# Performance work log

Hardware: AMD Instinct MI355X
Metric: run time of the kernel (lower is better)

Reference implementation:

```python
import jax, jax.numpy as jnp
import numpy as np

B, T, D = 4, 4096, 256
N_SCALES, N_EXPERTS = 3, 4
KERNELS = [5, 9, 17]           # kernel bank, one group of N_EXPERTS experts per size
E = N_SCALES * N_EXPERTS       # 12 total experts
EPS = 1e-5


def _dw_causal_conv(x, w):
    """Depthwise causal conv over time. x:[B,T,D], w:[k,D] -> [B,T,D]."""
    k = w.shape[0]
    xp = jnp.pad(x, ((0, 0), (k - 1, 0), (0, 0)))
    return jax.lax.conv_general_dilated(
        xp, w[:, None, :], window_strides=(1,), padding='VALID',
        dimension_numbers=('NWC', 'WIO', 'NWC'), feature_group_count=x.shape[-1])


def setup_inputs() -> dict:
    key = jax.random.key(0)
    ks = jax.random.split(key, 12)
    s = 0.02
    return {
        'x':       jax.random.normal(ks[0], (B, T, D), jnp.float32),
        'conv_k5':  jax.random.normal(ks[1], (N_EXPERTS, 5, D), jnp.float32) * s,
        'conv_k9':  jax.random.normal(ks[2], (N_EXPERTS, 9, D), jnp.float32) * s,
        'conv_k17': jax.random.normal(ks[3], (N_EXPERTS, 17, D), jnp.float32) * s,
        'proj_W':   jax.random.normal(ks[4], (E, D, D), jnp.float32) * s,
        'proj_b':   jnp.zeros((E, D), jnp.float32),
        'router_W': jax.random.normal(ks[5], (D, E), jnp.float32) * s,
        'router_b': jnp.zeros((E,), jnp.float32),
        'out_W':    jax.random.normal(ks[6], (D, D), jnp.float32) * s,
        'out_b':    jnp.zeros((D,), jnp.float32),
        'gamma':    jnp.ones((D,), jnp.float32),
        'beta':     jnp.zeros((D,), jnp.float32),
    }


def reference(x, conv_k5, conv_k9, conv_k17, proj_W, proj_b,
              router_W, router_b, out_W, out_b, gamma, beta):
    # per-scale expert SSM (causal depthwise conv), vmapped over the 4 experts per size
    ssm_out = jnp.concatenate([
        jax.vmap(lambda w: _dw_causal_conv(x, w))(conv_k5),
        jax.vmap(lambda w: _dw_causal_conv(x, w))(conv_k9),
        jax.vmap(lambda w: _dw_causal_conv(x, w))(conv_k17),
    ], axis=0)                                             # [E,B,T,D]
    # per-expert linear projection -> [B,T,E,D]
    stack = jnp.einsum('ebtd,edf->btef', ssm_out, proj_W) + proj_b
    # router: convex combination over E experts per token
    weights = jax.nn.softmax(x @ router_W + router_b, axis=-1)   # [B,T,E]
    mixed = jnp.einsum('btef,bte->btf', stack, weights)          # [B,T,D]
    # LayerNorm
    mu = jnp.mean(mixed, axis=-1, keepdims=True)
    var = jnp.var(mixed, axis=-1, keepdims=True)
    normed = (mixed - mu) * jax.lax.rsqrt(var + EPS) * gamma + beta
    return normed @ out_W + out_b
```

## Files before the change

### kernel.cpp

```cpp
#include <hip/hip_runtime.h>
#include <hip/hip_bf16.h>

typedef short short8 __attribute__((ext_vector_type(8)));
typedef short short4_t __attribute__((ext_vector_type(4)));
typedef float floatx4 __attribute__((ext_vector_type(4)));

#define DEVI __device__ __forceinline__


DEVI float bf2f(__hip_bfloat16 v) { return __bfloat162float(v); }
DEVI __hip_bfloat16 f2bf(float v) { return __float2bfloat16(v); }
DEVI unsigned short bfbits(float v) { __hip_bfloat16 b = f2bf(v); return *(unsigned short*)&b; }

__global__ __launch_bounds__(256) void prep_kernel(
    const float* __restrict__ rW,
    const float* __restrict__ projW,
    const float* __restrict__ outW,
    const float* __restrict__ projb,
    __hip_bfloat16* __restrict__ projWT,
    __hip_bfloat16* __restrict__ outWT,
    __hip_bfloat16* __restrict__ projbT,
    __hip_bfloat16* __restrict__ rWT)
{
    __shared__ __align__(16) __hip_bfloat16 Tt[64 * 72];
    const int bid = blockIdx.x;
    const int tid = threadIdx.x;

    if (bid == 208) {
#pragma unroll
        for (int k = 0; k < 32; k++)
            projbT[tid * 32 + k] = (k < 12) ? f2bf(projb[k * 256 + tid]) : f2bf(0.f);
#pragma unroll
        for (int e = 0; e < 16; e++)
            rWT[e * 256 + tid] = (e < 12) ? f2bf(rW[tid * 12 + e]) : f2bf(0.f);
        return;
    }
    const float* src;
    __hip_bfloat16* dst;
    if (bid < 192) {
        int e = bid >> 4, ti = (bid & 15) >> 2, tj = bid & 3;
        src = projW + (e << 16) + (ti * 64) * 256 + tj * 64;
        dst = projWT + (e << 16) + (tj * 64) * 256 + ti * 64;
    } else {
        int b3 = bid - 192, ti = b3 >> 2, tj = b3 & 3;
        src = outW + (ti * 64) * 256 + tj * 64;
        dst = outWT + (tj * 64) * 256 + ti * 64;
    }
#pragma unroll
    for (int i = 0; i < 4; i++) {
        int r = i * 16 + (tid >> 4);
        int c4 = (tid & 15) * 4;
        float4 f = *(const float4*)(src + r * 256 + c4);
        Tt[(c4 + 0) * 72 + r] = f2bf(f.x);
        Tt[(c4 + 1) * 72 + r] = f2bf(f.y);
        Tt[(c4 + 2) * 72 + r] = f2bf(f.z);
        Tt[(c4 + 3) * 72 + r] = f2bf(f.w);
    }
    __syncthreads();
#pragma unroll
    for (int i = 0; i < 2; i++) {
        int c = i * 32 + (tid >> 3);
        int r8 = (tid & 7) * 8;
        *(short8*)(dst + c * 256 + r8) = *(const short8*)(Tt + c * 72 + r8);
    }
}


template<int K>
DEVI void conv_reg(const float2 (&cf)[17], const unsigned (&xr)[32],
                   const float4 (&wt4)[4], unsigned* __restrict__ dp)
{
    constexpr int OFF = 17 - K;
#pragma unroll
    for (int t = 0; t < 16; t++) {
        float y0 = 0.f, y1 = 0.f;
#pragma unroll
        for (int i = 0; i < K; i++) {
            unsigned u = xr[t + OFF + i];
            y0 = fmaf(cf[i].x, __uint_as_float(u << 16), y0);
            y1 = fmaf(cf[i].y, __uint_as_float(u & 0xffff0000u), y1);
        }
        float wt = wt4[t >> 2][t & 3];
        unsigned pv = ((unsigned)bfbits(y1 * wt) << 16) | (unsigned)bfbits(y0 * wt);
        dp[t * 132] = pv;
    }
}

template<int NKS>
DEVI void gemm_pre(const __hip_bfloat16* __restrict__ A, int astride,
                   const short8 (&B)[4][2], floatx4 (&acc)[4][2],
                   int l16, int quad)
{
    const __hip_bfloat16* ap = A + l16 * astride + quad * 8;
    short8 a[4];
#pragma unroll
    for (int mf = 0; mf < 4; mf++) a[mf] = *(const short8*)(ap + mf * 16 * astride);
#pragma unroll
    for (int ks = 0; ks < NKS; ks++) {
        short8 na[4];
        if (ks < NKS - 1) {
#pragma unroll
            for (int mf = 0; mf < 4; mf++)
                na[mf] = *(const short8*)(ap + mf * 16 * astride + (ks + 1) * 32);
        }
#pragma unroll
        for (int nt = 0; nt < 2; nt++)
#pragma unroll
            for (int mf = 0; mf < 4; mf++)
                acc[mf][nt] = __builtin_amdgcn_mfma_f32_16x16x32_bf16(
                    a[mf], B[ks][nt], acc[mf][nt], 0, 0, 0);
        if (ks < NKS - 1) {
#pragma unroll
            for (int mf = 0; mf < 4; mf++) a[mf] = na[mf];
        }
    }
}

__global__ __launch_bounds__(512, 1) void fused_kernel(
    const float* __restrict__ x,
    const float* __restrict__ ck5, const float* __restrict__ ck9,
    const float* __restrict__ ck17,
    const float* __restrict__ rb,
    const float* __restrict__ gmm, const float* __restrict__ bta,
    const float* __restrict__ outb,
    const __hip_bfloat16* __restrict__ projWT,
    const __hip_bfloat16* __restrict__ outWT,
    const __hip_bfloat16* __restrict__ projbT,
    const __hip_bfloat16* __restrict__ rWT,
    float* __restrict__ out)
{
    __shared__ __align__(16) char smem[50432];
    __hip_bfloat16* xs = (__hip_bfloat16*)smem;
    __hip_bfloat16* As = (__hip_bfloat16*)smem;
    __hip_bfloat16* normed = (__hip_bfloat16*)smem;
    float* wts_s = (float*)(smem + 42240);
    float* psum  = (float*)(smem + 45312);
    float* psq   = (float*)(smem + 47616);
    float* muA   = (float*)(smem + 49920);
    float* rsA   = (float*)(smem + 50176);

    const int tid  = threadIdx.x;
    const int wave = tid >> 6;
    const int lane = tid & 63;
    const int quad = lane >> 4;
    const int l16  = lane & 15;
    const int nsl  = wave * 32;
    const int m0   = blockIdx.x * 64;
    const int bb   = m0 >> 12;
    const int t0   = m0 & 4095;

    {
        const float* xb = x + (size_t)bb * 4096 * 256;
        for (int idx = tid; idx < 80 * 64; idx += 512) {
            int row = idx >> 6, c4 = (idx & 63) << 2;
            int gt = t0 - 16 + row;
            short4_t v = {0, 0, 0, 0};
            if (gt >= 0) {
                float4 f = *(const float4*)(xb + (size_t)gt * 256 + c4);
                v[0] = (short)bfbits(f.x); v[1] = (short)bfbits(f.y);
                v[2] = (short)bfbits(f.z); v[3] = (short)bfbits(f.w);
            }
            *(short4_t*)(xs + row * 264 + c4) = v;
        }
    }
    __syncthreads();

    if (wave < 4) {
        floatx4 ra = {0.f, 0.f, 0.f, 0.f};
        const __hip_bfloat16* ap = xs + (16 + wave * 16 + l16) * 264 + quad * 8;
        const __hip_bfloat16* bp = rWT + l16 * 256 + quad * 8;
#pragma unroll
        for (int kk = 0; kk < 256; kk += 32)
            ra = __builtin_amdgcn_mfma_f32_16x16x32_bf16(
                *(const short8*)(ap + kk), *(const short8*)(bp + kk), ra, 0, 0, 0);
        float rbv = (l16 < 12) ? rb[l16] : 0.f;
#pragma unroll
        for (int r = 0; r < 4; r++) {
            float v = (l16 < 12) ? (ra[r] + rbv) : -1e30f;
            float mx = v;
            mx = fmaxf(mx, __shfl_xor(mx, 1));
            mx = fmaxf(mx, __shfl_xor(mx, 2));
            mx = fmaxf(mx, __shfl_xor(mx, 4));
            mx = fmaxf(mx, __shfl_xor(mx, 8));
            float ex = (l16 < 12) ? __expf(v - mx) : 0.f;
            float sm = ex;
            sm += __shfl_xor(sm, 1);
            sm += __shfl_xor(sm, 2);
            sm += __shfl_xor(sm, 4);
            sm += __shfl_xor(sm, 8);
            if (l16 < 12) wts_s[l16 * 64 + (wave * 16 + quad * 4 + r)] = ex / sm;
        }
    }

    const int d0   = 2 * (tid & 127);
    const int tloc = (tid >> 7) * 16;
    unsigned xr[32];
#pragma unroll
    for (int j = 0; j < 32; j++)
        xr[j] = *(const unsigned*)(xs + (tloc + j) * 264 + d0);
    __syncthreads();

    auto loadCoef = [&](float2 (&cf)[17], int e) {
        if (e < 4) {
            const float* cw = ck5 + e * 5 * 256;
#pragma unroll
            for (int j = 0; j < 17; j++)
                cf[j] = (j < 5) ? *(const float2*)(cw + j * 256 + d0) : make_float2(0.f, 0.f);
        } else if (e < 8) {
            const float* cw = ck9 + (e - 4) * 9 * 256;
#pragma unroll
            for (int j = 0; j < 17; j++)
                cf[j] = (j < 9) ? *(const float2*)(cw + j * 256 + d0) : make_float2(0.f, 0.f);
        } else {
            const float* cw = ck17 + (e - 8) * 17 * 256;
#pragma unroll
            for (int j = 0; j < 17; j++)
                cf[j] = *(const float2*)(cw + j * 256 + d0);
        }
    };
    auto loadB8 = [&](short8 (&B)[4][2], const __hip_bfloat16* base, int rs, int kstep) {
#pragma unroll
        for (int ks = 0; ks < 4; ks++)
#pragma unroll
            for (int nt = 0; nt < 2; nt++)
                B[ks][nt] = *(const short8*)(base + nt * 16 * rs + ks * kstep);
    };
    auto produce = [&](int e, const float2 (&cf)[17]) {
        float4 wt4[4];
#pragma unroll
        for (int g = 0; g < 4; g++)
            wt4[g] = *(const float4*)(wts_s + e * 64 + tloc + 4 * g);
        unsigned* dp = (unsigned*)As + tloc * 132 + (d0 >> 1);
        if (e < 4)      conv_reg<5>(cf, xr, wt4, dp);
        else if (e < 8) conv_reg<9>(cf, xr, wt4, dp);
        else            conv_reg<17>(cf, xr, wt4, dp);
    };
    auto produceBias = [&]() {
        int t = tid >> 3, k4 = (tid & 7) * 4;
        short4_t v;
#pragma unroll
        for (int j = 0; j < 4; j++) {
            int k = k4 + j;
            v[j] = (k < 12) ? (short)bfbits(wts_s[k * 64 + t]) : (short)0;
        }
        *(short4_t*)(As + t * 264 + k4) = v;
    };

    floatx4 acc[4][2];
#pragma unroll
    for (int i = 0; i < 4; i++)
#pragma unroll
        for (int j = 0; j < 2; j++) acc[i][j] = {0.f, 0.f, 0.f, 0.f};

    float2 cf[17];
    short8 BA[4][2], BB[4][2];

    loadCoef(cf, 0);
    loadB8(BA, projWT + (0 << 16) + 0   + (nsl + l16) * 256 + quad * 8, 256, 32);
    loadB8(BB, projWT + (0 << 16) + 128 + (nsl + l16) * 256 + quad * 8, 256, 32);
    produce(0, cf);
    __syncthreads();

#pragma unroll 1
    for (int c = 0; c < 12; c++) {
        if (c < 11) loadCoef(cf, c + 1);
        gemm_pre<4>(As, 264, BA, acc, l16, quad);
        gemm_pre<4>(As + 128, 264, BB, acc, l16, quad);
        if (c < 11) {
            int e = c + 1;
            loadB8(BA, projWT + (e << 16) + 0   + (nsl + l16) * 256 + quad * 8, 256, 32);
            loadB8(BB, projWT + (e << 16) + 128 + (nsl + l16) * 256 + quad * 8, 256, 32);
        } else {
            loadB8(BA, projbT + (nsl + l16) * 32 + quad * 8, 32, 0);
        }
        __syncthreads();
        if (c < 11) produce(c + 1, cf);
        else        produceBias();
        __syncthreads();
    }
    gemm_pre<1>(As, 264, BA, acc, l16, quad);

    loadB8(BA, outWT + 0   + (nsl + l16) * 256 + quad * 8, 256, 32);
    loadB8(BB, outWT + 128 + (nsl + l16) * 256 + quad * 8, 256, 32);

    {
        float s[16], s2[16];
#pragma unroll
        for (int mf = 0; mf < 4; mf++)
#pragma unroll
            for (int r = 0; r < 4; r++) {
                int i = mf * 4 + r;
                float v = 0.f, q = 0.f;
#pragma unroll
                for (int nt = 0; nt < 2; nt++) {
                    float a = acc[mf][nt][r];
                    v += a; q += a * a;
                }
                s[i] = v; s2[i] = q;
            }
#pragma unroll
        for (int m = 1; m <= 8; m <<= 1)
#pragma unroll
            for (int i = 0; i < 16; i++) {
                s[i]  += __shfl_xor(s[i], m);
                s2[i] += __shfl_xor(s2[i], m);
            }
#pragma unroll
        for (int i = 0; i < 16; i++)
            if (l16 == i) {
                int row = (i >> 2) * 16 + quad * 4 + (i & 3);
                psum[row * 9 + wave] = s[i];
                psq[row * 9 + wave]  = s2[i];
            }
    }
    __syncthreads();
    if (tid < 64) {
        float ss = 0.f, qq = 0.f;
#pragma unroll
        for (int p = 0; p < 8; p++) { ss += psum[tid * 9 + p]; qq += psq[tid * 9 + p]; }
        float mu = ss * 0.00390625f;
        float var = fmaxf(qq * 0.00390625f - mu * mu, 0.f);
        muA[tid] = mu;
        rsA[tid] = rsqrtf(var + 1e-5f);
    }
    __syncthreads();

#pragma unroll
    for (int nt = 0; nt < 2; nt++) {
        int col = nsl + nt * 16 + l16;
        float g = gmm[col], bt = bta[col];
#pragma unroll
        for (int mf = 0; mf < 4; mf++)
#pragma unroll
            for (int r = 0; r < 4; r++) {
                int row = mf * 16 + quad * 4 + r;
                normed[row * 264 + col] =
                    f2bf((acc[mf][nt][r] - muA[row]) * rsA[row] * g + bt);
            }
    }
    __syncthreads();

    floatx4 acc2[4][2];
#pragma unroll
    for (int i = 0; i < 4; i++)
#pragma unroll
        for (int j = 0; j < 2; j++) acc2[i][j] = {0.f, 0.f, 0.f, 0.f};
    gemm_pre<4>(normed, 264, BA, acc2, l16, quad);
    gemm_pre<4>(normed + 128, 264, BB, acc2, l16, quad);

    float* op = out + (size_t)m0 * 256;
#pragma unroll
    for (int nt = 0; nt < 2; nt++) {
        int col = nsl + nt * 16 + l16;
        float ob = outb[col];
#pragma unroll
        for (int mf = 0; mf < 4; mf++)
#pragma unroll
            for (int r = 0; r < 4; r++) {
                int row = mf * 16 + quad * 4 + r;
                op[row * 256 + col] = acc2[mf][nt][r] + ob;
            }
    }
}

extern "C" void kernel_launch(void* const* d_in, const int* in_sizes, int n_in,
                              void* d_out, int out_size, void* d_ws, size_t ws_size,
                              hipStream_t stream)
{
    (void)in_sizes; (void)n_in; (void)out_size; (void)ws_size;
    const float* x     = (const float*)d_in[0];
    const float* ck5   = (const float*)d_in[1];
    const float* ck9   = (const float*)d_in[2];
    const float* ck17  = (const float*)d_in[3];
    const float* projW = (const float*)d_in[4];
    const float* projb = (const float*)d_in[5];
    const float* rW    = (const float*)d_in[6];
    const float* rb    = (const float*)d_in[7];
    const float* outW  = (const float*)d_in[8];
    const float* outb  = (const float*)d_in[9];
    const float* gmm   = (const float*)d_in[10];
    const float* bta   = (const float*)d_in[11];

    __hip_bfloat16* projWT = (__hip_bfloat16*)d_ws;
    __hip_bfloat16* outWT  = (__hip_bfloat16*)((char*)d_ws + 1572864);
    __hip_bfloat16* projbT = (__hip_bfloat16*)((char*)d_ws + 1703936);
    __hip_bfloat16* rWT    = (__hip_bfloat16*)((char*)d_ws + 1720320);

    prep_kernel<<<dim3(209), dim3(256), 0, stream>>>(
        rW, projW, outW, projb, projWT, outWT, projbT, rWT);
    fused_kernel<<<dim3(256), dim3(512), 0, stream>>>(
        x, ck5, ck9, ck17, rb, gmm, bta, outb,
        projWT, outWT, projbT, rWT, (float*)d_out);
}
```

Baseline: 165.6 us.

## Double-buffer expert activations and interleave conv production with MFMA GEMM

Replaces the single shared activation buffer with two ping-pong buffers. While MFMAs consume the current expert's conv output, the conv for the next expert is computed and written into the other buffer. Each expert step now needs one barrier instead of two, and VALU conv work is interleaved with matrix ops. In exchange, dynamic shared memory grows to about 84 KB and register pressure rises, and the kernel now depends on setting the dynamic-LDS attribute.

```diff
diff --git a/kernel.cpp b/kernel.cpp
--- a/kernel.cpp
+++ b/kernel.cpp
@@ -65,6 +65,7 @@
     }
 }
 
+constexpr int SMEM_BYTES = 84224;
 
 template<int K>
 DEVI void conv_reg(const float2 (&cf)[17], const unsigned (&xr)[32],
@@ -83,6 +84,57 @@
         float wt = wt4[t >> 2][t & 3];
         unsigned pv = ((unsigned)bfbits(y1 * wt) << 16) | (unsigned)bfbits(y0 * wt);
         dp[t * 132] = pv;
+    }
+}
+
+template<int K>
+DEVI void chunk_fused(const __hip_bfloat16* __restrict__ bufC,
+                      unsigned* __restrict__ dpN,
+                      const short8 (&BA)[4][2], const short8 (&BB)[4][2],
+                      floatx4 (&acc)[4][2],
+                      const float2 (&cf)[17], const unsigned (&xr)[32],
+                      const float4 (&wt4)[4],
+                      int l16, int quad)
+{
+    constexpr int OFF = 17 - K;
+    const __hip_bfloat16* ap = bufC + l16 * 264 + quad * 8;
+    short8 a[4];
+#pragma unroll
+    for (int mf = 0; mf < 4; mf++) a[mf] = *(const short8*)(ap + mf * 16 * 264);
+#pragma unroll
+    for (int ks = 0; ks < 8; ks++) {
+#pragma unroll
+        for (int j = 0; j < 2; j++) {
+            int t = 2 * ks + j;
+            float y0 = 0.f, y1 = 0.f;
+#pragma unroll
+            for (int i = 0; i < K; i++) {
+                unsigned u = xr[t + OFF + i];
+                y0 = fmaf(cf[i].x, __uint_as_float(u << 16), y0);
+                y1 = fmaf(cf[i].y, __uint_as_float(u & 0xffff0000u), y1);
+            }
+            float wt = wt4[t >> 2][t & 3];
+            unsigned pv = ((unsigned)bfbits(y1 * wt) << 16) | (unsigned)bfbits(y0 * wt);
+            dpN[t * 132] = pv;
+        }
+        short8 na[4];
+        if (ks < 7) {
+#pragma unroll
+            for (int mf = 0; mf < 4; mf++)
+                na[mf] = *(const short8*)(ap + mf * 16 * 264 + (ks + 1) * 32);
+        }
+#pragma unroll
+        for (int nt = 0; nt < 2; nt++) {
+            short8 b = (ks < 4) ? BA[ks][nt] : BB[ks - 4][nt];
+#pragma unroll
+            for (int mf = 0; mf < 4; mf++)
+                acc[mf][nt] = __builtin_amdgcn_mfma_f32_16x16x32_bf16(
+                    a[mf], b, acc[mf][nt], 0, 0, 0);
+        }
+        if (ks < 7) {
+#pragma unroll
+            for (int mf = 0; mf < 4; mf++) a[mf] = na[mf];
+        }
     }
 }
 
@@ -129,15 +181,15 @@
     const __hip_bfloat16* __restrict__ rWT,
     float* __restrict__ out)
 {
-    __shared__ __align__(16) char smem[50432];
-    __hip_bfloat16* xs = (__hip_bfloat16*)smem;
-    __hip_bfloat16* As = (__hip_bfloat16*)smem;
-    __hip_bfloat16* normed = (__hip_bfloat16*)smem;
-    float* wts_s = (float*)(smem + 42240);
-    float* psum  = (float*)(smem + 45312);
-    float* psq   = (float*)(smem + 47616);
-    float* muA   = (float*)(smem + 49920);
-    float* rsA   = (float*)(smem + 50176);
+    extern __shared__ char smem[];
+    __hip_bfloat16* xs   = (__hip_bfloat16*)smem;
+    __hip_bfloat16* bufA = (__hip_bfloat16*)smem;
+    __hip_bfloat16* bufB = (__hip_bfloat16*)(smem + 42240);
+    float* wts_s = (float*)(smem + 76032);
+    float* psum  = (float*)(smem + 79104);
+    float* psq   = (float*)(smem + 81408);
+    float* muA   = (float*)(smem + 83712);
+    float* rsA   = (float*)(smem + 83968);
 
     const int tid  = threadIdx.x;
     const int wave = tid >> 6;
@@ -225,17 +277,12 @@
             for (int nt = 0; nt < 2; nt++)
                 B[ks][nt] = *(const short8*)(base + nt * 16 * rs + ks * kstep);
     };
-    auto produce = [&](int e, const float2 (&cf)[17]) {
-        float4 wt4[4];
+    auto loadWt = [&](float4 (&w)[4], int e) {
 #pragma unroll
         for (int g = 0; g < 4; g++)
-            wt4[g] = *(const float4*)(wts_s + e * 64 + tloc + 4 * g);
-        unsigned* dp = (unsigned*)As + tloc * 132 + (d0 >> 1);
-        if (e < 4)      conv_reg<5>(cf, xr, wt4, dp);
-        else if (e < 8) conv_reg<9>(cf, xr, wt4, dp);
-        else            conv_reg<17>(cf, xr, wt4, dp);
+            w[g] = *(const float4*)(wts_s + e * 64 + tloc + 4 * g);
     };
-    auto produceBias = [&]() {
+    auto produceBias = [&](__hip_bfloat16* dst) {
         int t = tid >> 3, k4 = (tid & 7) * 4;
         short4_t v;
 #pragma unroll
@@ -243,7 +290,7 @@
             int k = k4 + j;
             v[j] = (k < 12) ? (short)bfbits(wts_s[k * 64 + t]) : (short)0;
         }
-        *(short4_t*)(As + t * 264 + k4) = v;
+        *(short4_t*)(dst + t * 264 + k4) = v;
     };
 
     floatx4 acc[4][2];
@@ -254,33 +301,50 @@
 
     float2 cf[17];
     short8 BA[4][2], BB[4][2];
+    __hip_bfloat16* bufC = bufA;
+    __hip_bfloat16* bufN = bufB;
 
     loadCoef(cf, 0);
-    loadB8(BA, projWT + (0 << 16) + 0   + (nsl + l16) * 256 + quad * 8, 256, 32);
-    loadB8(BB, projWT + (0 << 16) + 128 + (nsl + l16) * 256 + quad * 8, 256, 32);
-    produce(0, cf);
-    __syncthreads();
+    loadB8(BA, projWT + (nsl + l16) * 256 + quad * 8, 256, 32);
+    loadB8(BB, projWT + 128 + (nsl + l16) * 256 + quad * 8, 256, 32);
+    {
+        float4 wt4[4];
+        loadWt(wt4, 0);
+        unsigned* dp = (unsigned*)bufC + tloc * 132 + (d0 >> 1);
+        conv_reg<5>(cf, xr, wt4, dp);
+    }
+    __syncthreads();
+
+#define REGION(KP, EXPERT)                                                      \
+    {                                                                           \
+        const int e_ = (EXPERT);                                                \
+        loadCoef(cf, e_);                                                       \
+        float4 wt4[4];                                                          \
+        loadWt(wt4, e_);                                                        \
+        unsigned* dpN = (unsigned*)bufN + tloc * 132 + (d0 >> 1);               \
+        chunk_fused<KP>(bufC, dpN, BA, BB, acc, cf, xr, wt4, l16, quad);        \
+        loadB8(BA, projWT + ((size_t)e_ << 16) + (nsl + l16) * 256 + quad * 8, 256, 32); \
+        loadB8(BB, projWT + ((size_t)e_ << 16) + 128 + (nsl + l16) * 256 + quad * 8, 256, 32); \
+        { __hip_bfloat16* t_ = bufC; bufC = bufN; bufN = t_; }                  \
+        __syncthreads();                                                        \
+    }
 
 #pragma unroll 1
-    for (int c = 0; c < 12; c++) {
-        if (c < 11) loadCoef(cf, c + 1);
-        gemm_pre<4>(As, 264, BA, acc, l16, quad);
-        gemm_pre<4>(As + 128, 264, BB, acc, l16, quad);
-        if (c < 11) {
-            int e = c + 1;
-            loadB8(BA, projWT + (e << 16) + 0   + (nsl + l16) * 256 + quad * 8, 256, 32);
-            loadB8(BB, projWT + (e << 16) + 128 + (nsl + l16) * 256 + quad * 8, 256, 32);
-        } else {
-            loadB8(BA, projbT + (nsl + l16) * 32 + quad * 8, 32, 0);
-        }
-        __syncthreads();
-        if (c < 11) produce(c + 1, cf);
-        else        produceBias();
-        __syncthreads();
-    }
-    gemm_pre<1>(As, 264, BA, acc, l16, quad);
-
-    loadB8(BA, outWT + 0   + (nsl + l16) * 256 + quad * 8, 256, 32);
+    for (int r = 0; r < 3; r++)  REGION(5,  r + 1)
+#pragma unroll 1
+    for (int r = 3; r < 7; r++)  REGION(9,  r + 1)
+#pragma unroll 1
+    for (int r = 7; r < 11; r++) REGION(17, r + 1)
+#undef REGION
+
+    produceBias(bufN);
+    gemm_pre<4>(bufC, 264, BA, acc, l16, quad);
+    gemm_pre<4>(bufC + 128, 264, BB, acc, l16, quad);
+    loadB8(BA, projbT + (nsl + l16) * 32 + quad * 8, 32, 0);
+    __syncthreads();
+    gemm_pre<1>(bufN, 264, BA, acc, l16, quad);
+
+    loadB8(BA, outWT + (nsl + l16) * 256 + quad * 8, 256, 32);
     loadB8(BB, outWT + 128 + (nsl + l16) * 256 + quad * 8, 256, 32);
 
     {
@@ -325,6 +389,7 @@
     }
     __syncthreads();
 
+    __hip_bfloat16* normed = bufC;
 #pragma unroll
     for (int nt = 0; nt < 2; nt++) {
         int col = nsl + nt * 16 + l16;
@@ -386,9 +451,16 @@
     __hip_bfloat16* projbT = (__hip_bfloat16*)((char*)d_ws + 1703936);
     __hip_bfloat16* rWT    = (__hip_bfloat16*)((char*)d_ws + 1720320);
 
+    static bool attr_set = false;
+    if (!attr_set) {
+        hipFuncSetAttribute((const void*)fused_kernel,
+                            hipFuncAttributeMaxDynamicSharedMemorySize, SMEM_BYTES);
+        attr_set = true;
+    }
+
     prep_kernel<<<dim3(209), dim3(256), 0, stream>>>(
         rW, projW, outW, projb, projWT, outWT, projbT, rWT);
-    fused_kernel<<<dim3(256), dim3(512), 0, stream>>>(
+    fused_kernel<<<dim3(256), dim3(512), SMEM_BYTES, stream>>>(
         x, ck5, ck9, ck17, rb, gmm, bta, outb,
         projWT, outWT, projbT, rWT, (float*)d_out);
 }
```

After: 168.9 us. 2.0% more time.

## Double-buffer expert conv tiles and split waves between GEMM-first and conv-first order

Applied to the files above, without the earlier changes.

The per-expert loop now keeps the conv output in two LDS buffers and ping-pongs between them, so the conv for expert r+1 can overlap the MFMA GEMM for expert r. Half the waves issue the GEMM first and the other half issue the conv first, which staggers MFMA and VALU work. The conv now reads x from LDS through a sliding register window instead of holding 32 preloaded registers, and GEMM B operands stream from global memory inside the k-loop instead of being fully preloaded. Dynamic shared memory grows to about 118 KB, and the extra global B loads in the inner loop may add latency.

```diff
diff --git a/kernel.cpp b/kernel.cpp
--- a/kernel.cpp
+++ b/kernel.cpp
@@ -65,53 +65,70 @@
     }
 }
 
+constexpr int SMEM_BYTES = 118016;
 
 template<int K>
-DEVI void conv_reg(const float2 (&cf)[17], const unsigned (&xr)[32],
-                   const float4 (&wt4)[4], unsigned* __restrict__ dp)
+DEVI void conv_lds2(const float2 (&cf)[17], const unsigned* __restrict__ xsu,
+                    int tloc, int du, const float4 (&wt4)[4],
+                    unsigned* __restrict__ dp)
 {
-    constexpr int OFF = 17 - K;
+    unsigned w[16];
+#pragma unroll
+    for (int i = 0; i < K - 1; i++)
+        w[i] = xsu[(16 + tloc - (K - 1) + i) * 132 + du];
 #pragma unroll
     for (int t = 0; t < 16; t++) {
-        float y0 = 0.f, y1 = 0.f;
-#pragma unroll
-        for (int i = 0; i < K; i++) {
-            unsigned u = xr[t + OFF + i];
-            y0 = fmaf(cf[i].x, __uint_as_float(u << 16), y0);
-            y1 = fmaf(cf[i].y, __uint_as_float(u & 0xffff0000u), y1);
+        unsigned nv = xsu[(16 + tloc + t) * 132 + du];
+        float y0 = cf[K - 1].x * __uint_as_float(nv << 16);
+        float y1 = cf[K - 1].y * __uint_as_float(nv & 0xffff0000u);
+#pragma unroll
+        for (int i = 0; i < K - 1; i++) {
+            y0 = fmaf(cf[i].x, __uint_as_float(w[i] << 16), y0);
+            y1 = fmaf(cf[i].y, __uint_as_float(w[i] & 0xffff0000u), y1);
         }
         float wt = wt4[t >> 2][t & 3];
         unsigned pv = ((unsigned)bfbits(y1 * wt) << 16) | (unsigned)bfbits(y0 * wt);
         dp[t * 132] = pv;
+#pragma unroll
+        for (int i = 0; i + 1 < K - 1; i++) w[i] = w[i + 1];
+        if (K > 1) w[K - 2] = nv;
     }
 }
 
 template<int NKS>
-DEVI void gemm_pre(const __hip_bfloat16* __restrict__ A, int astride,
-                   const short8 (&B)[4][2], floatx4 (&acc)[4][2],
-                   int l16, int quad)
+DEVI void gemm_inl(const __hip_bfloat16* __restrict__ A, int astride,
+                   const __hip_bfloat16* __restrict__ Bg, int bstride,
+                   floatx4 (&acc)[4][2], int l16, int quad, int nsl)
 {
     const __hip_bfloat16* ap = A + l16 * astride + quad * 8;
-    short8 a[4];
+    const __hip_bfloat16* bp = Bg + (nsl + l16) * bstride + quad * 8;
+    short8 a[4], b[2];
 #pragma unroll
     for (int mf = 0; mf < 4; mf++) a[mf] = *(const short8*)(ap + mf * 16 * astride);
 #pragma unroll
+    for (int nt = 0; nt < 2; nt++) b[nt] = *(const short8*)(bp + nt * 16 * bstride);
+#pragma unroll
     for (int ks = 0; ks < NKS; ks++) {
-        short8 na[4];
+        short8 na[4], nb[2];
         if (ks < NKS - 1) {
 #pragma unroll
             for (int mf = 0; mf < 4; mf++)
                 na[mf] = *(const short8*)(ap + mf * 16 * astride + (ks + 1) * 32);
+#pragma unroll
+            for (int nt = 0; nt < 2; nt++)
+                nb[nt] = *(const short8*)(bp + nt * 16 * bstride + (ks + 1) * 32);
         }
 #pragma unroll
         for (int nt = 0; nt < 2; nt++)
 #pragma unroll
             for (int mf = 0; mf < 4; mf++)
                 acc[mf][nt] = __builtin_amdgcn_mfma_f32_16x16x32_bf16(
-                    a[mf], B[ks][nt], acc[mf][nt], 0, 0, 0);
+                    a[mf], b[nt], acc[mf][nt], 0, 0, 0);
         if (ks < NKS - 1) {
 #pragma unroll
             for (int mf = 0; mf < 4; mf++) a[mf] = na[mf];
+#pragma unroll
+            for (int nt = 0; nt < 2; nt++) b[nt] = nb[nt];
         }
     }
 }
@@ -129,15 +146,16 @@
     const __hip_bfloat16* __restrict__ rWT,
     float* __restrict__ out)
 {
-    __shared__ __align__(16) char smem[50432];
-    __hip_bfloat16* xs = (__hip_bfloat16*)smem;
-    __hip_bfloat16* As = (__hip_bfloat16*)smem;
-    __hip_bfloat16* normed = (__hip_bfloat16*)smem;
-    float* wts_s = (float*)(smem + 42240);
-    float* psum  = (float*)(smem + 45312);
-    float* psq   = (float*)(smem + 47616);
-    float* muA   = (float*)(smem + 49920);
-    float* rsA   = (float*)(smem + 50176);
+    extern __shared__ char smem[];
+    __hip_bfloat16* xs   = (__hip_bfloat16*)smem;
+    __hip_bfloat16* bufA = (__hip_bfloat16*)(smem + 42240);
+    __hip_bfloat16* bufB = (__hip_bfloat16*)(smem + 76032);
+    float* wts_s = (float*)(smem + 109824);
+    float* psum  = (float*)(smem + 112896);
+    float* psq   = (float*)(smem + 115200);
+    float* muA   = (float*)(smem + 117504);
+    float* rsA   = (float*)(smem + 117760);
+    const unsigned* xsu = (const unsigned*)xs;
 
     const int tid  = threadIdx.x;
     const int wave = tid >> 6;
@@ -145,6 +163,7 @@
     const int quad = lane >> 4;
     const int l16  = lane & 15;
     const int nsl  = wave * 32;
+    const bool gemmFirst = (wave >= 4);
     const int m0   = blockIdx.x * 64;
     const int bb   = m0 >> 12;
     const int t0   = m0 & 4095;
@@ -191,14 +210,11 @@
             if (l16 < 12) wts_s[l16 * 64 + (wave * 16 + quad * 4 + r)] = ex / sm;
         }
     }
+    __syncthreads();
 
     const int d0   = 2 * (tid & 127);
+    const int du   = d0 >> 1;
     const int tloc = (tid >> 7) * 16;
-    unsigned xr[32];
-#pragma unroll
-    for (int j = 0; j < 32; j++)
-        xr[j] = *(const unsigned*)(xs + (tloc + j) * 264 + d0);
-    __syncthreads();
 
     auto loadCoef = [&](float2 (&cf)[17], int e) {
         if (e < 4) {
@@ -218,24 +234,19 @@
                 cf[j] = *(const float2*)(cw + j * 256 + d0);
         }
     };
-    auto loadB8 = [&](short8 (&B)[4][2], const __hip_bfloat16* base, int rs, int kstep) {
-#pragma unroll
-        for (int ks = 0; ks < 4; ks++)
-#pragma unroll
-            for (int nt = 0; nt < 2; nt++)
-                B[ks][nt] = *(const short8*)(base + nt * 16 * rs + ks * kstep);
-    };
-    auto produce = [&](int e, const float2 (&cf)[17]) {
+    auto produce = [&](int e, __hip_bfloat16* dst) {
+        float2 cf[17];
+        loadCoef(cf, e);
         float4 wt4[4];
 #pragma unroll
         for (int g = 0; g < 4; g++)
             wt4[g] = *(const float4*)(wts_s + e * 64 + tloc + 4 * g);
-        unsigned* dp = (unsigned*)As + tloc * 132 + (d0 >> 1);
-        if (e < 4)      conv_reg<5>(cf, xr, wt4, dp);
-        else if (e < 8) conv_reg<9>(cf, xr, wt4, dp);
-        else            conv_reg<17>(cf, xr, wt4, dp);
+        unsigned* dp = (unsigned*)dst + tloc * 132 + du;
+        if (e < 4)      conv_lds2<5>(cf, xsu, tloc, du, wt4, dp);
+        else if (e < 8) conv_lds2<9>(cf, xsu, tloc, du, wt4, dp);
+        else            conv_lds2<17>(cf, xsu, tloc, du, wt4, dp);
     };
-    auto produceBias = [&]() {
+    auto produceBias = [&](__hip_bfloat16* dst) {
         int t = tid >> 3, k4 = (tid & 7) * 4;
         short4_t v;
 #pragma unroll
@@ -243,7 +254,7 @@
             int k = k4 + j;
             v[j] = (k < 12) ? (short)bfbits(wts_s[k * 64 + t]) : (short)0;
         }
-        *(short4_t*)(As + t * 264 + k4) = v;
+        *(short4_t*)(dst + t * 264 + k4) = v;
     };
 
     floatx4 acc[4][2];
@@ -252,36 +263,38 @@
 #pragma unroll
         for (int j = 0; j < 2; j++) acc[i][j] = {0.f, 0.f, 0.f, 0.f};
 
-    float2 cf[17];
-    short8 BA[4][2], BB[4][2];
-
-    loadCoef(cf, 0);
-    loadB8(BA, projWT + (0 << 16) + 0   + (nsl + l16) * 256 + quad * 8, 256, 32);
-    loadB8(BB, projWT + (0 << 16) + 128 + (nsl + l16) * 256 + quad * 8, 256, 32);
-    produce(0, cf);
+    __hip_bfloat16* bufC = bufA;
+    __hip_bfloat16* bufN = bufB;
+
+    produce(0, bufC);
     __syncthreads();
 
 #pragma unroll 1
-    for (int c = 0; c < 12; c++) {
-        if (c < 11) loadCoef(cf, c + 1);
-        gemm_pre<4>(As, 264, BA, acc, l16, quad);
-        gemm_pre<4>(As + 128, 264, BB, acc, l16, quad);
-        if (c < 11) {
-            int e = c + 1;
-            loadB8(BA, projWT + (e << 16) + 0   + (nsl + l16) * 256 + quad * 8, 256, 32);
-            loadB8(BB, projWT + (e << 16) + 128 + (nsl + l16) * 256 + quad * 8, 256, 32);
+    for (int r = 0; r < 11; r++) {
+        const __hip_bfloat16* Bg = projWT + ((size_t)r << 16);
+        if (gemmFirst) {
+            gemm_inl<8>(bufC, 264, Bg, 256, acc, l16, quad, nsl);
+            produce(r + 1, bufN);
         } else {
-            loadB8(BA, projbT + (nsl + l16) * 32 + quad * 8, 32, 0);
-        }
+            produce(r + 1, bufN);
+            gemm_inl<8>(bufC, 264, Bg, 256, acc, l16, quad, nsl);
+        }
+        { __hip_bfloat16* t_ = bufC; bufC = bufN; bufN = t_; }
         __syncthreads();
-        if (c < 11) produce(c + 1, cf);
-        else        produceBias();
+    }
+    {
+        const __hip_bfloat16* Bg = projWT + ((size_t)11 << 16);
+        if (gemmFirst) {
+            gemm_inl<8>(bufC, 264, Bg, 256, acc, l16, quad, nsl);
+            produceBias(bufN);
+        } else {
+            produceBias(bufN);
+            gemm_inl<8>(bufC, 264, Bg, 256, acc, l16, quad, nsl);
+        }
+        { __hip_bfloat16* t_ = bufC; bufC = bufN; bufN = t_; }
         __syncthreads();
     }
-    gemm_pre<1>(As, 264, BA, acc, l16, quad);
-
-    loadB8(BA, outWT + 0   + (nsl + l16) * 256 + quad * 8, 256, 32);
-    loadB8(BB, outWT + 128 + (nsl + l16) * 256 + quad * 8, 256, 32);
+    gemm_inl<1>(bufC, 264, projbT, 32, acc, l16, quad, nsl);
 
     {
         float s[16], s2[16];
@@ -325,6 +338,7 @@
     }
     __syncthreads();
 
+    __hip_bfloat16* normed = bufN;
 #pragma unroll
     for (int nt = 0; nt < 2; nt++) {
         int col = nsl + nt * 16 + l16;
@@ -345,8 +359,7 @@
     for (int i = 0; i < 4; i++)
 #pragma unroll
         for (int j = 0; j < 2; j++) acc2[i][j] = {0.f, 0.f, 0.f, 0.f};
-    gemm_pre<4>(normed, 264, BA, acc2, l16, quad);
-    gemm_pre<4>(normed + 128, 264, BB, acc2, l16, quad);
+    gemm_inl<8>(normed, 264, outWT, 256, acc2, l16, quad, nsl);
 
     float* op = out + (size_t)m0 * 256;
 #pragma unroll
@@ -386,9 +399,16 @@
     __hip_bfloat16* projbT = (__hip_bfloat16*)((char*)d_ws + 1703936);
     __hip_bfloat16* rWT    = (__hip_bfloat16*)((char*)d_ws + 1720320);
 
+    static bool attr_set = false;
+    if (!attr_set) {
+        hipFuncSetAttribute((const void*)fused_kernel,
+                            hipFuncAttributeMaxDynamicSharedMemorySize, SMEM_BYTES);
+        attr_set = true;
+    }
+
     prep_kernel<<<dim3(209), dim3(256), 0, stream>>>(
         rW, projW, outW, projb, projWT, outWT, projbT, rWT);
-    fused_kernel<<<dim3(256), dim3(512), 0, stream>>>(
+    fused_kernel<<<dim3(256), dim3(512), SMEM_BYTES, stream>>>(
         x, ck5, ck9, ck17, rb, gmm, bta, outb,
         projWT, outWT, projbT, rWT, (float*)d_out);
 }
```

After: 174.6 us. +5.5%, slower.

## Stream projection weights into double-buffered LDS via async global-to-LDS loads

Applied to the files above, without the earlier changes.

Projection weights are pre-tiled and XOR-swizzled into 64-column K-chunks, then streamed into two LDS buffers with global_load_lds while the MFMA loop consumes the other buffer. Each expert's GEMM is split into four sub-steps, so weight fetch overlaps compute and the large per-thread B register arrays go away. The output GEMM now reads B straight from global memory, and the bf16 packing uses v_cvt_pk_bf16_f32. The cost is about twice the LDS footprint plus extra barriers per sub-step.

```diff
diff --git a/kernel.cpp b/kernel.cpp
--- a/kernel.cpp
+++ b/kernel.cpp
@@ -11,13 +11,19 @@
 DEVI float bf2f(__hip_bfloat16 v) { return __bfloat162float(v); }
 DEVI __hip_bfloat16 f2bf(float v) { return __float2bfloat16(v); }
 DEVI unsigned short bfbits(float v) { __hip_bfloat16 b = f2bf(v); return *(unsigned short*)&b; }
+
+typedef __attribute__((address_space(3))) void lds_void_t;
+typedef const __attribute__((address_space(1))) void gbl_void_t;
+DEVI void gload16(const void* g, void* l) {
+    __builtin_amdgcn_global_load_lds((gbl_void_t*)g, (lds_void_t*)l, 16, 0, 0);
+}
 
 __global__ __launch_bounds__(256) void prep_kernel(
     const float* __restrict__ rW,
     const float* __restrict__ projW,
     const float* __restrict__ outW,
     const float* __restrict__ projb,
-    __hip_bfloat16* __restrict__ projWT,
+    __hip_bfloat16* __restrict__ projS,
     __hip_bfloat16* __restrict__ outWT,
     __hip_bfloat16* __restrict__ projbT,
     __hip_bfloat16* __restrict__ rWT)
@@ -36,35 +42,54 @@
         return;
     }
     const float* src;
-    __hip_bfloat16* dst;
     if (bid < 192) {
         int e = bid >> 4, ti = (bid & 15) >> 2, tj = bid & 3;
         src = projW + (e << 16) + (ti * 64) * 256 + tj * 64;
-        dst = projWT + (e << 16) + (tj * 64) * 256 + ti * 64;
+#pragma unroll
+        for (int i = 0; i < 4; i++) {
+            int r = i * 16 + (tid >> 4);
+            int c4 = (tid & 15) * 4;
+            float4 f = *(const float4*)(src + r * 256 + c4);
+            Tt[(c4 + 0) * 72 + r] = f2bf(f.x);
+            Tt[(c4 + 1) * 72 + r] = f2bf(f.y);
+            Tt[(c4 + 2) * 72 + r] = f2bf(f.z);
+            Tt[(c4 + 3) * 72 + r] = f2bf(f.w);
+        }
+        __syncthreads();
+#pragma unroll
+        for (int i = 0; i < 2; i++) {
+            int ff = i * 32 + (tid >> 3);
+            int g8 = (tid & 7) * 8;
+            int f = tj * 64 + ff;
+            size_t dst = ((size_t)((bid >> 4) * 4 + ti) * 256 + f) * 64
+                         + (g8 ^ ((f & 7) << 3));
+            *(short8*)(projS + dst) = *(const short8*)(Tt + ff * 72 + g8);
+        }
     } else {
         int b3 = bid - 192, ti = b3 >> 2, tj = b3 & 3;
         src = outW + (ti * 64) * 256 + tj * 64;
-        dst = outWT + (tj * 64) * 256 + ti * 64;
-    }
-#pragma unroll
-    for (int i = 0; i < 4; i++) {
-        int r = i * 16 + (tid >> 4);
-        int c4 = (tid & 15) * 4;
-        float4 f = *(const float4*)(src + r * 256 + c4);
-        Tt[(c4 + 0) * 72 + r] = f2bf(f.x);
-        Tt[(c4 + 1) * 72 + r] = f2bf(f.y);
-        Tt[(c4 + 2) * 72 + r] = f2bf(f.z);
-        Tt[(c4 + 3) * 72 + r] = f2bf(f.w);
-    }
-    __syncthreads();
-#pragma unroll
-    for (int i = 0; i < 2; i++) {
-        int c = i * 32 + (tid >> 3);
-        int r8 = (tid & 7) * 8;
-        *(short8*)(dst + c * 256 + r8) = *(const short8*)(Tt + c * 72 + r8);
-    }
-}
-
+        __hip_bfloat16* dst = outWT + (tj * 64) * 256 + ti * 64;
+#pragma unroll
+        for (int i = 0; i < 4; i++) {
+            int r = i * 16 + (tid >> 4);
+            int c4 = (tid & 15) * 4;
+            float4 f = *(const float4*)(src + r * 256 + c4);
+            Tt[(c4 + 0) * 72 + r] = f2bf(f.x);
+            Tt[(c4 + 1) * 72 + r] = f2bf(f.y);
+            Tt[(c4 + 2) * 72 + r] = f2bf(f.z);
+            Tt[(c4 + 3) * 72 + r] = f2bf(f.w);
+        }
+        __syncthreads();
+#pragma unroll
+        for (int i = 0; i < 2; i++) {
+            int c = i * 32 + (tid >> 3);
+            int r8 = (tid & 7) * 8;
+            *(short8*)(dst + c * 256 + r8) = *(const short8*)(Tt + c * 72 + r8);
+        }
+    }
+}
+
+constexpr int SMEM_BYTES = 107520;
 
 template<int K>
 DEVI void conv_reg(const float2 (&cf)[17], const unsigned (&xr)[32],
@@ -81,37 +106,45 @@
             y1 = fmaf(cf[i].y, __uint_as_float(u & 0xffff0000u), y1);
         }
         float wt = wt4[t >> 2][t & 3];
-        unsigned pv = ((unsigned)bfbits(y1 * wt) << 16) | (unsigned)bfbits(y0 * wt);
+        unsigned pv;
+        asm("v_cvt_pk_bf16_f32 %0, %1, %2" : "=v"(pv) : "v"(y0 * wt), "v"(y1 * wt));
         dp[t * 132] = pv;
     }
 }
 
-template<int NKS>
-DEVI void gemm_pre(const __hip_bfloat16* __restrict__ A, int astride,
-                   const short8 (&B)[4][2], floatx4 (&acc)[4][2],
-                   int l16, int quad)
+DEVI void gemm_out(const __hip_bfloat16* __restrict__ A,
+                   const __hip_bfloat16* __restrict__ Bg,
+                   floatx4 (&acc)[4][2], int l16, int quad, int nsl)
 {
-    const __hip_bfloat16* ap = A + l16 * astride + quad * 8;
-    short8 a[4];
-#pragma unroll
-    for (int mf = 0; mf < 4; mf++) a[mf] = *(const short8*)(ap + mf * 16 * astride);
-#pragma unroll
-    for (int ks = 0; ks < NKS; ks++) {
-        short8 na[4];
-        if (ks < NKS - 1) {
+    const __hip_bfloat16* ap = A + l16 * 264 + quad * 8;
+    const __hip_bfloat16* bp = Bg + (nsl + l16) * 256 + quad * 8;
+    short8 a[4], b[2];
+#pragma unroll
+    for (int mf = 0; mf < 4; mf++) a[mf] = *(const short8*)(ap + mf * 16 * 264);
+#pragma unroll
+    for (int nt = 0; nt < 2; nt++) b[nt] = *(const short8*)(bp + nt * 16 * 256);
+#pragma unroll
+    for (int ks = 0; ks < 8; ks++) {
+        short8 na[4], nb[2];
+        if (ks < 7) {
 #pragma unroll
             for (int mf = 0; mf < 4; mf++)
-                na[mf] = *(const short8*)(ap + mf * 16 * astride + (ks + 1) * 32);
+                na[mf] = *(const short8*)(ap + mf * 16 * 264 + (ks + 1) * 32);
+#pragma unroll
+            for (int nt = 0; nt < 2; nt++)
+                nb[nt] = *(const short8*)(bp + nt * 16 * 256 + (ks + 1) * 32);
         }
 #pragma unroll
         for (int nt = 0; nt < 2; nt++)
 #pragma unroll
             for (int mf = 0; mf < 4; mf++)
                 acc[mf][nt] = __builtin_amdgcn_mfma_f32_16x16x32_bf16(
-                    a[mf], B[ks][nt], acc[mf][nt], 0, 0, 0);
-        if (ks < NKS - 1) {
+                    a[mf], b[nt], acc[mf][nt], 0, 0, 0);
+        if (ks < 7) {
 #pragma unroll
             for (int mf = 0; mf < 4; mf++) a[mf] = na[mf];
+#pragma unroll
+            for (int nt = 0; nt < 2; nt++) b[nt] = nb[nt];
         }
     }
 }
@@ -123,21 +156,23 @@
     const float* __restrict__ rb,
     const float* __restrict__ gmm, const float* __restrict__ bta,
     const float* __restrict__ outb,
-    const __hip_bfloat16* __restrict__ projWT,
+    const __hip_bfloat16* __restrict__ projS,
     const __hip_bfloat16* __restrict__ outWT,
     const __hip_bfloat16* __restrict__ projbT,
     const __hip_bfloat16* __restrict__ rWT,
     float* __restrict__ out)
 {
-    __shared__ __align__(16) char smem[50432];
+    extern __shared__ char smem[];
+    __hip_bfloat16* Bls0 = (__hip_bfloat16*)smem;
+    __hip_bfloat16* Bls1 = (__hip_bfloat16*)(smem + 32768);
+    __hip_bfloat16* As   = (__hip_bfloat16*)(smem + 65536);
+    float* wts_s = (float*)(smem + 99328);
+    float* psum  = (float*)(smem + 102400);
+    float* psq   = (float*)(smem + 104704);
+    float* muA   = (float*)(smem + 107008);
+    float* rsA   = (float*)(smem + 107264);
     __hip_bfloat16* xs = (__hip_bfloat16*)smem;
-    __hip_bfloat16* As = (__hip_bfloat16*)smem;
-    __hip_bfloat16* normed = (__hip_bfloat16*)smem;
-    float* wts_s = (float*)(smem + 42240);
-    float* psum  = (float*)(smem + 45312);
-    float* psq   = (float*)(smem + 47616);
-    float* muA   = (float*)(smem + 49920);
-    float* rsA   = (float*)(smem + 50176);
+    __hip_bfloat16* normed = As;
 
     const int tid  = threadIdx.x;
     const int wave = tid >> 6;
@@ -193,6 +228,7 @@
     }
 
     const int d0   = 2 * (tid & 127);
+    const int du   = d0 >> 1;
     const int tloc = (tid >> 7) * 16;
     unsigned xr[32];
 #pragma unroll
@@ -218,19 +254,14 @@
                 cf[j] = *(const float2*)(cw + j * 256 + d0);
         }
     };
-    auto loadB8 = [&](short8 (&B)[4][2], const __hip_bfloat16* base, int rs, int kstep) {
-#pragma unroll
-        for (int ks = 0; ks < 4; ks++)
-#pragma unroll
-            for (int nt = 0; nt < 2; nt++)
-                B[ks][nt] = *(const short8*)(base + nt * 16 * rs + ks * kstep);
-    };
-    auto produce = [&](int e, const float2 (&cf)[17]) {
+    auto produceE = [&](int e) {
+        float2 cf[17];
+        loadCoef(cf, e);
         float4 wt4[4];
 #pragma unroll
         for (int g = 0; g < 4; g++)
             wt4[g] = *(const float4*)(wts_s + e * 64 + tloc + 4 * g);
-        unsigned* dp = (unsigned*)As + tloc * 132 + (d0 >> 1);
+        unsigned* dp = (unsigned*)As + tloc * 132 + du;
         if (e < 4)      conv_reg<5>(cf, xr, wt4, dp);
         else if (e < 8) conv_reg<9>(cf, xr, wt4, dp);
         else            conv_reg<17>(cf, xr, wt4, dp);
@@ -245,6 +276,36 @@
         }
         *(short4_t*)(As + t * 264 + k4) = v;
     };
+    auto issueB = [&](int cc2, int buf) {
+        const char* g = (const char*)projS
+            + (((size_t)cc2 * 256 + wave * 32) << 7) + lane * 16;
+        char* lb = (char*)(buf ? Bls1 : Bls0) + ((wave * 32) << 7);
+#pragma unroll
+        for (int i = 0; i < 4; i++)
+            gload16(g + i * 1024, lb + i * 1024);
+    };
+    auto gemm_sub = [&](int sub, const __hip_bfloat16* B, floatx4 (&acc)[4][2]) {
+        const __hip_bfloat16* ap = As + l16 * 264 + sub * 64 + quad * 8;
+        const int swz = (l16 & 7) << 3;
+        const int bbase = (nsl + l16) * 64;
+#pragma unroll
+        for (int ks = 0; ks < 2; ks++) {
+            int joff = ((ks << 5) | (quad << 3)) ^ swz;
+            short8 a[4], b[2];
+#pragma unroll
+            for (int mf = 0; mf < 4; mf++)
+                a[mf] = *(const short8*)(ap + mf * 16 * 264 + ks * 32);
+#pragma unroll
+            for (int nt = 0; nt < 2; nt++)
+                b[nt] = *(const short8*)(B + bbase + nt * 1024 + joff);
+#pragma unroll
+            for (int nt = 0; nt < 2; nt++)
+#pragma unroll
+                for (int mf = 0; mf < 4; mf++)
+                    acc[mf][nt] = __builtin_amdgcn_mfma_f32_16x16x32_bf16(
+                        a[mf], b[nt], acc[mf][nt], 0, 0, 0);
+        }
+    };
 
     floatx4 acc[4][2];
 #pragma unroll
@@ -252,36 +313,41 @@
 #pragma unroll
         for (int j = 0; j < 2; j++) acc[i][j] = {0.f, 0.f, 0.f, 0.f};
 
-    float2 cf[17];
-    short8 BA[4][2], BB[4][2];
-
-    loadCoef(cf, 0);
-    loadB8(BA, projWT + (0 << 16) + 0   + (nsl + l16) * 256 + quad * 8, 256, 32);
-    loadB8(BB, projWT + (0 << 16) + 128 + (nsl + l16) * 256 + quad * 8, 256, 32);
-    produce(0, cf);
-    __syncthreads();
-
+    issueB(0, 0);
+    produceE(0);
+    __syncthreads();
+
+    int cur = 0;
 #pragma unroll 1
-    for (int c = 0; c < 12; c++) {
-        if (c < 11) loadCoef(cf, c + 1);
-        gemm_pre<4>(As, 264, BA, acc, l16, quad);
-        gemm_pre<4>(As + 128, 264, BB, acc, l16, quad);
-        if (c < 11) {
-            int e = c + 1;
-            loadB8(BA, projWT + (e << 16) + 0   + (nsl + l16) * 256 + quad * 8, 256, 32);
-            loadB8(BB, projWT + (e << 16) + 128 + (nsl + l16) * 256 + quad * 8, 256, 32);
+    for (int cc = 0; cc < 48; ++cc) {
+        const int e = cc >> 2, sub = cc & 3;
+        if (cc < 47) issueB(cc + 1, cur ^ 1);
+        gemm_sub(sub, cur ? Bls1 : Bls0, acc);
+        if (sub == 3) {
+            __syncthreads();
+            if (e < 11) produceE(e + 1);
+            else        produceBias();
+            __syncthreads();
         } else {
-            loadB8(BA, projbT + (nsl + l16) * 32 + quad * 8, 32, 0);
-        }
-        __syncthreads();
-        if (c < 11) produce(c + 1, cf);
-        else        produceBias();
-        __syncthreads();
-    }
-    gemm_pre<1>(As, 264, BA, acc, l16, quad);
-
-    loadB8(BA, outWT + 0   + (nsl + l16) * 256 + quad * 8, 256, 32);
-    loadB8(BB, outWT + 128 + (nsl + l16) * 256 + quad * 8, 256, 32);
+            __syncthreads();
+        }
+        cur ^= 1;
+    }
+    {
+        const __hip_bfloat16* ap = As + l16 * 264 + quad * 8;
+        const __hip_bfloat16* bp = projbT + (nsl + l16) * 32 + quad * 8;
+        short8 a[4], b[2];
+#pragma unroll
+        for (int mf = 0; mf < 4; mf++) a[mf] = *(const short8*)(ap + mf * 16 * 264);
+#pragma unroll
+        for (int nt = 0; nt < 2; nt++) b[nt] = *(const short8*)(bp + nt * 16 * 32);
+#pragma unroll
+        for (int nt = 0; nt < 2; nt++)
+#pragma unroll
+            for (int mf = 0; mf < 4; mf++)
+                acc[mf][nt] = __builtin_amdgcn_mfma_f32_16x16x32_bf16(
+                    a[mf], b[nt], acc[mf][nt], 0, 0, 0);
+    }
 
     {
         float s[16], s2[16];
@@ -345,8 +411,7 @@
     for (int i = 0; i < 4; i++)
 #pragma unroll
         for (int j = 0; j < 2; j++) acc2[i][j] = {0.f, 0.f, 0.f, 0.f};
-    gemm_pre<4>(normed, 264, BA, acc2, l16, quad);
-    gemm_pre<4>(normed + 128, 264, BB, acc2, l16, quad);
+    gemm_out(normed, outWT, acc2, l16, quad, nsl);
 
     float* op = out + (size_t)m0 * 256;
 #pragma unroll
@@ -381,14 +446,21 @@
     const float* gmm   = (const float*)d_in[10];
     const float* bta   = (const float*)d_in[11];
 
-    __hip_bfloat16* projWT = (__hip_bfloat16*)d_ws;
+    __hip_bfloat16* projS  = (__hip_bfloat16*)d_ws;
     __hip_bfloat16* outWT  = (__hip_bfloat16*)((char*)d_ws + 1572864);
     __hip_bfloat16* projbT = (__hip_bfloat16*)((char*)d_ws + 1703936);
     __hip_bfloat16* rWT    = (__hip_bfloat16*)((char*)d_ws + 1720320);
 
+    static bool attr_set = false;
+    if (!attr_set) {
+        hipFuncSetAttribute((const void*)fused_kernel,
+                            hipFuncAttributeMaxDynamicSharedMemorySize, SMEM_BYTES);
+        attr_set = true;
+    }
+
     prep_kernel<<<dim3(209), dim3(256), 0, stream>>>(
-        rW, projW, outW, projb, projWT, outWT, projbT, rWT);
-    fused_kernel<<<dim3(256), dim3(512), 0, stream>>>(
+        rW, projW, outW, projb, projS, outWT, projbT, rWT);
+    fused_kernel<<<dim3(256), dim3(512), SMEM_BYTES, stream>>>(
         x, ck5, ck9, ck17, rb, gmm, bta, outb,
-        projWT, outWT, projbT, rWT, (float*)d_out);
-}
+        projS, outWT, projbT, rWT, (float*)d_out);
+}
```

Measured after the change: 177.7 us. +7.3%, slower.
